# Kernel optimization log

Measured on AMD Instinct MI355X. Metric: run time of the kernel, lower is better.

The kernel has to match this reference:

```python
import jax, jax.numpy as jnp
import numpy as np

H = 1024          # hidden_size
E = 2 * H         # expansion e
S_DIM = 128       # shared q/k dim s
B, S = 4, 2048


def setup_inputs() -> dict:
    key = jax.random.key(0)
    ks = jax.random.split(key, 6)
    inputs = jax.random.normal(ks[0], (B, S, H), dtype=jnp.float32)
    W_uv = jax.random.normal(ks[1], (H, 2 * E + S_DIM), dtype=jnp.float32) * (1.0 / np.sqrt(H))
    b_uv = jnp.zeros((2 * E + S_DIM,), dtype=jnp.float32)
    gamma = jax.random.normal(ks[2], (2, S_DIM), dtype=jnp.float32) * 0.02
    beta = jnp.zeros((2, S_DIM), dtype=jnp.float32)
    W_out = jax.random.normal(ks[3], (E, H), dtype=jnp.float32) * (1.0 / np.sqrt(E))
    b_out = jnp.zeros((H,), dtype=jnp.float32)
    return {"inputs": inputs, "W_uv": W_uv, "b_uv": b_uv,
            "gamma": gamma, "beta": beta, "W_out": W_out, "b_out": b_out}


def reference(inputs, W_uv, b_uv, gamma, beta, W_out, b_out):
    seq_len = inputs.shape[1]
    # uv projection + SiLU
    uvb = jax.nn.silu(jnp.einsum('bsh,hf->bsf', inputs, W_uv) + b_uv)
    u = uvb[..., :E]                       # [B,S,E]
    v = uvb[..., E:2 * E]                  # [B,S,E]
    base = uvb[..., 2 * E:]                # [B,S,s]
    # per-head affine: [B,S,1,s]*[2,s] + [2,s] -> [B,S,2,s]
    qk = base[..., None, :] * gamma + beta
    q, k = qk[..., 0, :], qk[..., 1, :]    # [B,S,s] each
    scores = jnp.einsum('bns,bms->bnm', q, k) / seq_len   # [B,S,S]
    sq = jnp.square(jax.nn.relu(scores))
    attn_v = jnp.einsum('bnm,bme->bne', sq, v)            # [B,S,E]
    return jnp.einsum('bne,eh->bnh', u * attn_v, W_out) + b_out
```

## Files before the change

kernel.cpp:

```cpp
#include <hip/hip_runtime.h>
#include <stdint.h>


#define H_DIM  1024
#define E_DIM  2048
#define SD     128
#define B_SZ   4
#define S_LEN  2048
#define M_TOT  (B_SZ * S_LEN)
#define F_DIM  (2 * E_DIM + SD)

typedef _Float16 f16;
typedef __attribute__((ext_vector_type(4))) _Float16 f16x4;
typedef __attribute__((ext_vector_type(8))) _Float16 f16x8;
typedef __attribute__((ext_vector_type(16))) float f32x16;

__device__ __forceinline__ float silu_f(float x) { return x / (1.f + __expf(-x)); }

__device__ __forceinline__ void gload16(const void* g, void* l) {
  __builtin_amdgcn_global_load_lds(
      (const __attribute__((address_space(1))) void*)(uintptr_t)g,
      (__attribute__((address_space(3))) void*)(uint32_t)(uintptr_t)l,
      16, 0, 0);
}

__global__ __launch_bounds__(256) void cast_f16_k(const float* __restrict__ src,
                                                  f16* __restrict__ dst, long n) {
  long i = ((long)blockIdx.x * 256 + threadIdx.x) * 4;
  if (i < n) {
    float4 v = *(const float4*)(src + i);
    f16x4 h; h[0] = (f16)v.x; h[1] = (f16)v.y; h[2] = (f16)v.z; h[3] = (f16)v.w;
    *(f16x4*)(dst + i) = h;
  }
}

__global__ __launch_bounds__(256) void transpose_cast_k(const float* __restrict__ src,
                                                        f16* __restrict__ dst, int R, int C) {
  __shared__ float tile[32][33];
  int c0 = blockIdx.x * 32, r0 = blockIdx.y * 32;
  int tx = threadIdx.x & 31, ty = threadIdx.x >> 5;
  for (int i = ty; i < 32; i += 8) tile[i][tx] = src[(long)(r0 + i) * C + c0 + tx];
  __syncthreads();
  for (int i = ty; i < 32; i += 8) dst[(long)(c0 + i) * R + r0 + tx] = (f16)tile[tx][i];
}

template <int MODE>
__global__ __launch_bounds__(512, 2) void gemm256(
    const f16* __restrict__ Ag, const f16* __restrict__ Bg,
    float* __restrict__ F0, f16* __restrict__ O0, f16* __restrict__ O1,
    const f16* __restrict__ I0, const float* __restrict__ C0)
{
  constexpr int K  = (MODE == 0) ? H_DIM : (MODE == 1) ? SD : 2048;
  constexpr int NT = K / 64;

  __shared__ f16 As[2][256][64];
  __shared__ f16 Bs[2][256][64];

  const int t    = threadIdx.x;
  const int w    = t >> 6;
  const int lane = t & 63;
  const int lo5  = lane & 31;
  const int hi   = lane >> 5;
  const int wm   = w >> 2;
  const int wn   = w & 3;

  const int gx  = gridDim.x;
  const int nwg = gx * gridDim.y;
  const int lin = blockIdx.y * gx + blockIdx.x;
  const int cpx = nwg >> 3;
  const int wg  = (lin & 7) * cpx + (lin >> 3);
  const int n0  = (wg % gx) * 256;
  const int m0  = (wg / gx) * 256;
  const long z  = blockIdx.z;

  const f16* A = Ag + (MODE == 2 ? z * (long)S_LEN * S_LEN
                     : MODE == 1 ? z * (long)S_LEN * SD : 0);
  const f16* B = Bg + (MODE == 2 ? z * (long)E_DIM * S_LEN
                     : MODE == 1 ? z * (long)S_LEN * SD : 0);

  auto stageA = [&](int bb, int half, int kt2) {
    const f16* g0 = A + (long)(m0 + half * 128) * K + kt2 * 64;
    f16* lb = &As[bb][half * 128][0];
#pragma unroll
    for (int j = 0; j < 2; j++) {
      int grp = (j << 3) + w;
      int rl  = (grp << 3) + (lane >> 3);
      gload16(g0 + (long)rl * K + (((lane & 7) ^ (lane >> 3) ^ (grp & 1)) << 3),
              lb + (grp << 9));
    }
  };
  auto stageB = [&](int bb, int half, int kt2) {
    const f16* g0 = B + (long)(n0 + half * 128) * K + kt2 * 64;
    f16* lb = &Bs[bb][half * 128][0];
#pragma unroll
    for (int j = 0; j < 2; j++) {
      int grp = (j << 3) + w;
      int rl  = (grp << 3) + (lane >> 3);
      gload16(g0 + (long)rl * K + (((lane & 7) ^ (lane >> 3) ^ (grp & 1)) << 3),
              lb + (grp << 9));
    }
  };

  f32x16 acc[4][2] = {};
  f16x8 a0[2][4], a1[2][4], b0[4], b1[4];

  const int swz = (lo5 & 7) ^ ((lo5 >> 3) & 1);
  const int rA  = wm * 64 + lo5;
  const int rB  = wn * 32 + lo5;

  stageA(0, 0, 0); stageA(0, 1, 0); stageB(0, 0, 0); stageB(0, 1, 0);
  stageA(1, 0, 1); stageA(1, 1, 1); stageB(1, 0, 1); stageB(1, 1, 1);
  asm volatile("s_waitcnt vmcnt(8)" ::: "memory");
  __builtin_amdgcn_s_barrier();

  for (int kt = 0; kt < NT; ++kt) {
    const int bf = kt & 1;
    const bool s2 = (kt + 2 < NT);

#pragma unroll
    for (int ksl = 0; ksl < 4; ksl++) {
      const int pc = ((((ksl << 1) + hi) ^ swz) << 3);
      a0[0][ksl] = *(const f16x8*)&As[bf][rA][pc];
      a0[1][ksl] = *(const f16x8*)&As[bf][rA + 32][pc];
      b0[ksl]    = *(const f16x8*)&Bs[bf][rB][pc];
    }
    __builtin_amdgcn_s_barrier();
    __builtin_amdgcn_s_setprio(1);
#pragma unroll
    for (int ksl = 0; ksl < 4; ksl++) {
      acc[0][0] = __builtin_amdgcn_mfma_f32_32x32x16_f16(a0[0][ksl], b0[ksl], acc[0][0], 0, 0, 0);
      acc[0][1] = __builtin_amdgcn_mfma_f32_32x32x16_f16(a0[1][ksl], b0[ksl], acc[0][1], 0, 0, 0);
    }
    __builtin_amdgcn_s_setprio(0);
    __builtin_amdgcn_s_barrier();

    if (s2) { stageA(bf, 0, kt + 2); stageB(bf, 0, kt + 2); }
#pragma unroll
    for (int ksl = 0; ksl < 4; ksl++) {
      const int pc = ((((ksl << 1) + hi) ^ swz) << 3);
      b1[ksl] = *(const f16x8*)&Bs[bf][128 + rB][pc];
    }
    __builtin_amdgcn_s_barrier();
    __builtin_amdgcn_s_setprio(1);
#pragma unroll
    for (int ksl = 0; ksl < 4; ksl++) {
      acc[1][0] = __builtin_amdgcn_mfma_f32_32x32x16_f16(a0[0][ksl], b1[ksl], acc[1][0], 0, 0, 0);
      acc[1][1] = __builtin_amdgcn_mfma_f32_32x32x16_f16(a0[1][ksl], b1[ksl], acc[1][1], 0, 0, 0);
    }
    __builtin_amdgcn_s_setprio(0);
    __builtin_amdgcn_s_barrier();

    if (s2) stageB(bf, 1, kt + 2);
#pragma unroll
    for (int ksl = 0; ksl < 4; ksl++) {
      const int pc = ((((ksl << 1) + hi) ^ swz) << 3);
      a1[0][ksl] = *(const f16x8*)&As[bf][128 + rA][pc];
      a1[1][ksl] = *(const f16x8*)&As[bf][128 + rA + 32][pc];
    }
    __builtin_amdgcn_s_barrier();
    __builtin_amdgcn_s_setprio(1);
#pragma unroll
    for (int ksl = 0; ksl < 4; ksl++) {
      acc[3][0] = __builtin_amdgcn_mfma_f32_32x32x16_f16(a1[0][ksl], b1[ksl], acc[3][0], 0, 0, 0);
      acc[3][1] = __builtin_amdgcn_mfma_f32_32x32x16_f16(a1[1][ksl], b1[ksl], acc[3][1], 0, 0, 0);
    }
    __builtin_amdgcn_s_setprio(0);
    __builtin_amdgcn_s_barrier();

    if (s2) stageA(bf, 1, kt + 2);
    __builtin_amdgcn_s_barrier();
    __builtin_amdgcn_s_setprio(1);
#pragma unroll
    for (int ksl = 0; ksl < 4; ksl++) {
      acc[2][0] = __builtin_amdgcn_mfma_f32_32x32x16_f16(a1[0][ksl], b0[ksl], acc[2][0], 0, 0, 0);
      acc[2][1] = __builtin_amdgcn_mfma_f32_32x32x16_f16(a1[1][ksl], b0[ksl], acc[2][1], 0, 0, 0);
    }
    __builtin_amdgcn_s_setprio(0);
    if (s2) { asm volatile("s_waitcnt vmcnt(8)" ::: "memory"); }
    else    { asm volatile("s_waitcnt vmcnt(0)" ::: "memory"); }
    __builtin_amdgcn_s_barrier();
  }

#pragma unroll
  for (int q = 0; q < 4; q++) {
    const int ms = q >> 1;
    const int ns = q & 1;
#pragma unroll
    for (int im = 0; im < 2; im++) {
      const int gc    = n0 + ns * 128 + wn * 32 + lo5;
      const int rbase = m0 + ms * 128 + wm * 64 + im * 32 + (hi << 2);
      if (MODE == 0) {
        const float bias = C0[gc];
        if (n0 < E_DIM) {
#pragma unroll
          for (int g = 0; g < 4; g++)
#pragma unroll
            for (int rr = 0; rr < 4; rr++) {
              int gr = rbase + (g << 3) + rr;
              O0[(long)gr * E_DIM + gc] = (f16)silu_f(acc[q][im][g * 4 + rr] + bias);
            }
        } else {
#pragma unroll
          for (int g = 0; g < 4; g++) {
            int gr0 = rbase + (g << 3);
            int b   = gr0 >> 11;
            int s0  = gr0 & (S_LEN - 1);
            f16x4 pk;
#pragma unroll
            for (int rr = 0; rr < 4; rr++) pk[rr] = (f16)silu_f(acc[q][im][g * 4 + rr] + bias);
            *(f16x4*)&O1[((long)b * E_DIM + (gc - E_DIM)) * S_LEN + s0] = pk;
          }
        }
      } else if (MODE == 1) {
        const long base = z * (long)S_LEN * S_LEN;
#pragma unroll
        for (int g = 0; g < 4; g++)
#pragma unroll
          for (int rr = 0; rr < 4; rr++) {
            int gr = rbase + (g << 3) + rr;
            float tv = fmaxf(acc[q][im][g * 4 + rr], 0.f) * 64.f;
            O0[base + (long)gr * S_LEN + gc] = (f16)(tv * tv);
          }
      } else if (MODE == 2) {
        const long rowoff = z * S_LEN;
#pragma unroll
        for (int g = 0; g < 4; g++)
#pragma unroll
          for (int rr = 0; rr < 4; rr++) {
            int gr = rbase + (g << 3) + rr;
            long idx = (rowoff + gr) * (long)E_DIM + gc;
            O0[idx] = (f16)((float)I0[idx] * acc[q][im][g * 4 + rr]);
          }
      } else {
        const float bias = C0[gc];
#pragma unroll
        for (int g = 0; g < 4; g++)
#pragma unroll
          for (int rr = 0; rr < 4; rr++) {
            int gr = rbase + (g << 3) + rr;
            F0[(long)gr * H_DIM + gc] = acc[q][im][g * 4 + rr] * (1.0f / 17179869184.0f) + bias;
          }
      }
    }
  }
}

template <int MODE>
__global__ __launch_bounds__(256) void mfma_gemm(
    const f16* __restrict__ Ag, const f16* __restrict__ Bg,
    float* __restrict__ F0, f16* __restrict__ H0, const f16* __restrict__ H1,
    f16* __restrict__ H2, f16* __restrict__ H3,
    const float* __restrict__ C0, const float* __restrict__ C1,
    const float* __restrict__ C2)
{
  constexpr int K   = (MODE == 1) ? SD : H_DIM;
  constexpr int LDA = K, LDB = K;

  __shared__ f16 As[2][128][32];
  __shared__ f16 Bs[2][128][32];

  const int t    = threadIdx.x;
  const int w    = t >> 6;
  const int lane = t & 63;
  const int lo5  = lane & 31;
  const int hi   = lane >> 5;
  const int wy   = w >> 1, wx = w & 1;
  const int m0   = blockIdx.y * 128;
  const int n0   = blockIdx.x * 128;
  const long z   = blockIdx.z;

  const f16* A = Ag + (MODE == 1 ? z * (long)S_LEN * SD : 0);
  const f16* B = Bg + (MODE == 1 ? z * (long)S_LEN * SD : 0);

  const int srow = lane >> 2;
  const int scol = (((lane & 3) ^ ((srow >> 1) & 3))) * 8;
  const int rsw  = (lo5 >> 1) & 3;

  f32x16 acc[2][2] = {};

  for (int k0 = 0; k0 < K; k0 += 64) {
#pragma unroll
    for (int h = 0; h < 2; h++)
#pragma unroll
      for (int g16 = 0; g16 < 2; g16++) {
        const int r = (w << 5) + (g16 << 4);
        gload16(A + (long)(m0 + r + srow) * LDA + k0 + (h << 5) + scol, &As[h][r][0]);
        gload16(B + (long)(n0 + r + srow) * LDB + k0 + (h << 5) + scol, &Bs[h][r][0]);
      }
    __syncthreads();

#pragma unroll
    for (int ks = 0; ks < 4; ks++) {
      const int h  = ks >> 1;
      const int cl = ((ks & 1) << 1) + hi;
      const int kc = (cl ^ rsw) << 3;
      f16x8 av[2], bv[2];
#pragma unroll
      for (int i = 0; i < 2; i++)
        av[i] = *(const f16x8*)&As[h][(wy << 6) + (i << 5) + lo5][kc];
#pragma unroll
      for (int j = 0; j < 2; j++)
        bv[j] = *(const f16x8*)&Bs[h][(wx << 6) + (j << 5) + lo5][kc];
#pragma unroll
      for (int i = 0; i < 2; i++)
#pragma unroll
        for (int j = 0; j < 2; j++)
          acc[i][j] = __builtin_amdgcn_mfma_f32_32x32x16_f16(av[i], bv[j], acc[i][j], 0, 0, 0);
    }
    __syncthreads();
  }

  const int rb0 = m0 + (wy << 6) + (hi << 2);
  const int cb0 = n0 + (wx << 6) + lo5;

  if (MODE == 4) {
#pragma unroll
    for (int i = 0; i < 2; i++)
#pragma unroll
      for (int j = 0; j < 2; j++) {
        int jj = cb0 + (j << 5);
        float bias = C0[jj];
        float g0 = C1[jj], g1 = C1[SD + jj];
        float be0 = C2[jj], be1 = C2[SD + jj];
#pragma unroll
        for (int g = 0; g < 4; g++)
#pragma unroll
          for (int rr = 0; rr < 4; rr++) {
            int gr = rb0 + (i << 5) + (g << 3) + rr;
            float s = silu_f(acc[i][j][g * 4 + rr] + bias);
            H2[(long)gr * SD + jj] = (f16)(s * g0 + be0);
            H3[(long)gr * SD + jj] = (f16)(s * g1 + be1);
          }
      }
  } else {
#pragma unroll
    for (int i = 0; i < 2; i++)
#pragma unroll
      for (int j = 0; j < 2; j++) {
        int gc = cb0 + (j << 5);
#pragma unroll
        for (int g = 0; g < 4; g++)
#pragma unroll
          for (int rr = 0; rr < 4; rr++) {
            int gr = rb0 + (i << 5) + (g << 3) + rr;
            float tv = fmaxf(acc[i][j][g * 4 + rr], 0.f) * 64.f;
            H0[z * (long)S_LEN * S_LEN + (long)gr * S_LEN + gc] = (f16)(tv * tv);
          }
      }
  }
}

extern "C" void kernel_launch(void* const* d_in, const int* in_sizes, int n_in,
                              void* d_out, int out_size, void* d_ws, size_t ws_size,
                              hipStream_t stream) {
  const float* X     = (const float*)d_in[0];
  const float* W_uv  = (const float*)d_in[1];
  const float* b_uv  = (const float*)d_in[2];
  const float* gamma = (const float*)d_in[3];
  const float* beta  = (const float*)d_in[4];
  const float* W_out = (const float*)d_in[5];
  const float* b_out = (const float*)d_in[6];
  float* out = (float*)d_out;

  char* wp = (char*)d_ws;
  f16* Xh   = (f16*)wp; wp += (long)M_TOT * H_DIM * 2;
  f16* Wuvt = (f16*)wp; wp += (long)F_DIM * H_DIM * 2;
  f16* Wt   = (f16*)wp; wp += (long)H_DIM * E_DIM * 2;
  f16* u    = (f16*)wp; wp += (long)M_TOT * E_DIM * 2;
  f16* vt   = (f16*)wp; wp += (long)M_TOT * E_DIM * 2;
  f16* qh   = (f16*)wp; wp += (long)M_TOT * SD * 2;
  f16* kh   = (f16*)wp; wp += (long)M_TOT * SD * 2;
  f16* sq   = (f16*)wp; wp += (long)B_SZ * S_LEN * S_LEN * 2;
  f16* p    = (f16*)wp; wp += (long)M_TOT * E_DIM * 2;

  cast_f16_k<<<(M_TOT * H_DIM) / (256 * 4), 256, 0, stream>>>(X, Xh, (long)M_TOT * H_DIM);
  transpose_cast_k<<<dim3(F_DIM / 32, H_DIM / 32), 256, 0, stream>>>(W_uv, Wuvt, H_DIM, F_DIM);
  transpose_cast_k<<<dim3(H_DIM / 32, E_DIM / 32), 256, 0, stream>>>(W_out, Wt, E_DIM, H_DIM);

  gemm256<0><<<dim3(2 * E_DIM / 256, M_TOT / 256, 1), 512, 0, stream>>>(
      Xh, Wuvt, nullptr, u, vt, nullptr, b_uv);

  mfma_gemm<4><<<dim3(1, M_TOT / 128, 1), 256, 0, stream>>>(
      Xh, Wuvt + (long)2 * E_DIM * H_DIM, nullptr, nullptr, nullptr, qh, kh,
      b_uv + 2 * E_DIM, gamma, beta);

  gemm256<1><<<dim3(S_LEN / 256, S_LEN / 256, B_SZ), 512, 0, stream>>>(
      qh, kh, nullptr, sq, nullptr, nullptr, nullptr);

  gemm256<2><<<dim3(E_DIM / 256, S_LEN / 256, B_SZ), 512, 0, stream>>>(
      sq, vt, nullptr, p, nullptr, u, nullptr);

  gemm256<3><<<dim3(H_DIM / 256, M_TOT / 256, 1), 512, 0, stream>>>(
      p, Wt, out, nullptr, nullptr, nullptr, b_out);
}
```

Measured before the change: 384.9 us.

## Fuse q/k projection into uv GEMM and split-K the output GEMM

Extends the uv projection GEMM with an extra column tile that computes the shared base projection and writes q and k with the per-head affine. This removes the separate small-tile GEMM launch. The final output GEMM is split into two K halves across grid z: one half writes to the output with bias, the other to a scratch buffer. A vector add kernel then combines them. This fills more CUs in the final GEMM at the cost of an extra full-output read/write pass and wasted padding work in the extra tile.

```diff
diff --git a/kernel.cpp b/kernel.cpp
--- a/kernel.cpp
+++ b/kernel.cpp
@@ -44,14 +44,26 @@
   for (int i = ty; i < 32; i += 8) dst[(long)(c0 + i) * R + r0 + tx] = (f16)tile[tx][i];
 }
 
+__global__ __launch_bounds__(256) void addf4_k(float* __restrict__ dst,
+                                               const float* __restrict__ src) {
+  long i = ((long)blockIdx.x * 256 + threadIdx.x) * 4;
+  float4 a = *(const float4*)(dst + i);
+  float4 b = *(const float4*)(src + i);
+  a.x += b.x; a.y += b.y; a.z += b.z; a.w += b.w;
+  *(float4*)(dst + i) = a;
+}
+
 template <int MODE>
 __global__ __launch_bounds__(512, 2) void gemm256(
     const f16* __restrict__ Ag, const f16* __restrict__ Bg,
     float* __restrict__ F0, f16* __restrict__ O0, f16* __restrict__ O1,
-    const f16* __restrict__ I0, const float* __restrict__ C0)
+    const f16* __restrict__ I0, const float* __restrict__ C0,
+    const float* __restrict__ C1, const float* __restrict__ C2,
+    f16* __restrict__ Q0, f16* __restrict__ K0)
 {
-  constexpr int K  = (MODE == 0) ? H_DIM : (MODE == 1) ? SD : 2048;
-  constexpr int NT = K / 64;
+  constexpr int KE = (MODE == 0) ? H_DIM : (MODE == 1) ? SD : (MODE == 2) ? 2048 : 1024;
+  constexpr int LD = (MODE == 3) ? 2048 : KE;
+  constexpr int NT = KE / 64;
 
   __shared__ f16 As[2][256][64];
   __shared__ f16 Bs[2][256][64];
@@ -74,29 +86,33 @@
   const long z  = blockIdx.z;
 
   const f16* A = Ag + (MODE == 2 ? z * (long)S_LEN * S_LEN
-                     : MODE == 1 ? z * (long)S_LEN * SD : 0);
+                     : MODE == 1 ? z * (long)S_LEN * SD
+                     : MODE == 3 ? z * 1024 : 0);
   const f16* B = Bg + (MODE == 2 ? z * (long)E_DIM * S_LEN
-                     : MODE == 1 ? z * (long)S_LEN * SD : 0);
+                     : MODE == 1 ? z * (long)S_LEN * SD
+                     : MODE == 3 ? z * 1024 : 0);
 
   auto stageA = [&](int bb, int half, int kt2) {
-    const f16* g0 = A + (long)(m0 + half * 128) * K + kt2 * 64;
+    const f16* g0 = A + (long)(m0 + half * 128) * LD + kt2 * 64;
     f16* lb = &As[bb][half * 128][0];
 #pragma unroll
     for (int j = 0; j < 2; j++) {
       int grp = (j << 3) + w;
       int rl  = (grp << 3) + (lane >> 3);
-      gload16(g0 + (long)rl * K + (((lane & 7) ^ (lane >> 3) ^ (grp & 1)) << 3),
+      gload16(g0 + (long)rl * LD + (((lane & 7) ^ (lane >> 3) ^ (grp & 1)) << 3),
               lb + (grp << 9));
     }
   };
   auto stageB = [&](int bb, int half, int kt2) {
-    const f16* g0 = B + (long)(n0 + half * 128) * K + kt2 * 64;
     f16* lb = &Bs[bb][half * 128][0];
 #pragma unroll
     for (int j = 0; j < 2; j++) {
       int grp = (j << 3) + w;
       int rl  = (grp << 3) + (lane >> 3);
-      gload16(g0 + (long)rl * K + (((lane & 7) ^ (lane >> 3) ^ (grp & 1)) << 3),
+      int grow = n0 + half * 128 + rl;
+      if (MODE == 0) grow = min(grow, F_DIM - 1);
+      gload16(B + (long)grow * LD + kt2 * 64 +
+                  (((lane & 7) ^ (lane >> 3) ^ (grp & 1)) << 3),
               lb + (grp << 9));
     }
   };
@@ -190,8 +206,8 @@
       const int gc    = n0 + ns * 128 + wn * 32 + lo5;
       const int rbase = m0 + ms * 128 + wm * 64 + im * 32 + (hi << 2);
       if (MODE == 0) {
-        const float bias = C0[gc];
         if (n0 < E_DIM) {
+          const float bias = C0[gc];
 #pragma unroll
           for (int g = 0; g < 4; g++)
 #pragma unroll
@@ -199,7 +215,8 @@
               int gr = rbase + (g << 3) + rr;
               O0[(long)gr * E_DIM + gc] = (f16)silu_f(acc[q][im][g * 4 + rr] + bias);
             }
-        } else {
+        } else if (n0 < 2 * E_DIM) {
+          const float bias = C0[gc];
 #pragma unroll
           for (int g = 0; g < 4; g++) {
             int gr0 = rbase + (g << 3);
@@ -210,6 +227,22 @@
             for (int rr = 0; rr < 4; rr++) pk[rr] = (f16)silu_f(acc[q][im][g * 4 + rr] + bias);
             *(f16x4*)&O1[((long)b * E_DIM + (gc - E_DIM)) * S_LEN + s0] = pk;
           }
+        } else {
+          int jj = gc - 2 * E_DIM;
+          if (jj < SD) {
+            float bias = C0[gc];
+            float g0 = C1[jj], g1 = C1[SD + jj];
+            float be0 = C2[jj], be1 = C2[SD + jj];
+#pragma unroll
+            for (int g = 0; g < 4; g++)
+#pragma unroll
+              for (int rr = 0; rr < 4; rr++) {
+                int gr = rbase + (g << 3) + rr;
+                float s = silu_f(acc[q][im][g * 4 + rr] + bias);
+                Q0[(long)gr * SD + jj] = (f16)(s * g0 + be0);
+                K0[(long)gr * SD + jj] = (f16)(s * g1 + be1);
+              }
+          }
         }
       } else if (MODE == 1) {
         const long base = z * (long)S_LEN * S_LEN;
@@ -232,121 +265,17 @@
             O0[idx] = (f16)((float)I0[idx] * acc[q][im][g * 4 + rr]);
           }
       } else {
-        const float bias = C0[gc];
+        float* dst = (z == 0) ? F0 : (float*)O1;
+        const float bias = (z == 0) ? C0[gc] : 0.f;
 #pragma unroll
         for (int g = 0; g < 4; g++)
 #pragma unroll
           for (int rr = 0; rr < 4; rr++) {
             int gr = rbase + (g << 3) + rr;
-            F0[(long)gr * H_DIM + gc] = acc[q][im][g * 4 + rr] * (1.0f / 17179869184.0f) + bias;
+            dst[(long)gr * H_DIM + gc] = acc[q][im][g * 4 + rr] * (1.0f / 17179869184.0f) + bias;
           }
       }
     }
-  }
-}
-
-template <int MODE>
-__global__ __launch_bounds__(256) void mfma_gemm(
-    const f16* __restrict__ Ag, const f16* __restrict__ Bg,
-    float* __restrict__ F0, f16* __restrict__ H0, const f16* __restrict__ H1,
-    f16* __restrict__ H2, f16* __restrict__ H3,
-    const float* __restrict__ C0, const float* __restrict__ C1,
-    const float* __restrict__ C2)
-{
-  constexpr int K   = (MODE == 1) ? SD : H_DIM;
-  constexpr int LDA = K, LDB = K;
-
-  __shared__ f16 As[2][128][32];
-  __shared__ f16 Bs[2][128][32];
-
-  const int t    = threadIdx.x;
-  const int w    = t >> 6;
-  const int lane = t & 63;
-  const int lo5  = lane & 31;
-  const int hi   = lane >> 5;
-  const int wy   = w >> 1, wx = w & 1;
-  const int m0   = blockIdx.y * 128;
-  const int n0   = blockIdx.x * 128;
-  const long z   = blockIdx.z;
-
-  const f16* A = Ag + (MODE == 1 ? z * (long)S_LEN * SD : 0);
-  const f16* B = Bg + (MODE == 1 ? z * (long)S_LEN * SD : 0);
-
-  const int srow = lane >> 2;
-  const int scol = (((lane & 3) ^ ((srow >> 1) & 3))) * 8;
-  const int rsw  = (lo5 >> 1) & 3;
-
-  f32x16 acc[2][2] = {};
-
-  for (int k0 = 0; k0 < K; k0 += 64) {
-#pragma unroll
-    for (int h = 0; h < 2; h++)
-#pragma unroll
-      for (int g16 = 0; g16 < 2; g16++) {
-        const int r = (w << 5) + (g16 << 4);
-        gload16(A + (long)(m0 + r + srow) * LDA + k0 + (h << 5) + scol, &As[h][r][0]);
-        gload16(B + (long)(n0 + r + srow) * LDB + k0 + (h << 5) + scol, &Bs[h][r][0]);
-      }
-    __syncthreads();
-
-#pragma unroll
-    for (int ks = 0; ks < 4; ks++) {
-      const int h  = ks >> 1;
-      const int cl = ((ks & 1) << 1) + hi;
-      const int kc = (cl ^ rsw) << 3;
-      f16x8 av[2], bv[2];
-#pragma unroll
-      for (int i = 0; i < 2; i++)
-        av[i] = *(const f16x8*)&As[h][(wy << 6) + (i << 5) + lo5][kc];
-#pragma unroll
-      for (int j = 0; j < 2; j++)
-        bv[j] = *(const f16x8*)&Bs[h][(wx << 6) + (j << 5) + lo5][kc];
-#pragma unroll
-      for (int i = 0; i < 2; i++)
-#pragma unroll
-        for (int j = 0; j < 2; j++)
-          acc[i][j] = __builtin_amdgcn_mfma_f32_32x32x16_f16(av[i], bv[j], acc[i][j], 0, 0, 0);
-    }
-    __syncthreads();
-  }
-
-  const int rb0 = m0 + (wy << 6) + (hi << 2);
-  const int cb0 = n0 + (wx << 6) + lo5;
-
-  if (MODE == 4) {
-#pragma unroll
-    for (int i = 0; i < 2; i++)
-#pragma unroll
-      for (int j = 0; j < 2; j++) {
-        int jj = cb0 + (j << 5);
-        float bias = C0[jj];
-        float g0 = C1[jj], g1 = C1[SD + jj];
-        float be0 = C2[jj], be1 = C2[SD + jj];
-#pragma unroll
-        for (int g = 0; g < 4; g++)
-#pragma unroll
-          for (int rr = 0; rr < 4; rr++) {
-            int gr = rb0 + (i << 5) + (g << 3) + rr;
-            float s = silu_f(acc[i][j][g * 4 + rr] + bias);
-            H2[(long)gr * SD + jj] = (f16)(s * g0 + be0);
-            H3[(long)gr * SD + jj] = (f16)(s * g1 + be1);
-          }
-      }
-  } else {
-#pragma unroll
-    for (int i = 0; i < 2; i++)
-#pragma unroll
-      for (int j = 0; j < 2; j++) {
-        int gc = cb0 + (j << 5);
-#pragma unroll
-        for (int g = 0; g < 4; g++)
-#pragma unroll
-          for (int rr = 0; rr < 4; rr++) {
-            int gr = rb0 + (i << 5) + (g << 3) + rr;
-            float tv = fmaxf(acc[i][j][g * 4 + rr], 0.f) * 64.f;
-            H0[z * (long)S_LEN * S_LEN + (long)gr * S_LEN + gc] = (f16)(tv * tv);
-          }
-      }
   }
 }
 
@@ -377,19 +306,17 @@
   transpose_cast_k<<<dim3(F_DIM / 32, H_DIM / 32), 256, 0, stream>>>(W_uv, Wuvt, H_DIM, F_DIM);
   transpose_cast_k<<<dim3(H_DIM / 32, E_DIM / 32), 256, 0, stream>>>(W_out, Wt, E_DIM, H_DIM);
 
-  gemm256<0><<<dim3(2 * E_DIM / 256, M_TOT / 256, 1), 512, 0, stream>>>(
-      Xh, Wuvt, nullptr, u, vt, nullptr, b_uv);
-
-  mfma_gemm<4><<<dim3(1, M_TOT / 128, 1), 256, 0, stream>>>(
-      Xh, Wuvt + (long)2 * E_DIM * H_DIM, nullptr, nullptr, nullptr, qh, kh,
-      b_uv + 2 * E_DIM, gamma, beta);
+  gemm256<0><<<dim3(17, M_TOT / 256, 1), 512, 0, stream>>>(
+      Xh, Wuvt, nullptr, u, vt, nullptr, b_uv, gamma, beta, qh, kh);
 
   gemm256<1><<<dim3(S_LEN / 256, S_LEN / 256, B_SZ), 512, 0, stream>>>(
-      qh, kh, nullptr, sq, nullptr, nullptr, nullptr);
+      qh, kh, nullptr, sq, nullptr, nullptr, nullptr, nullptr, nullptr, nullptr, nullptr);
 
   gemm256<2><<<dim3(E_DIM / 256, S_LEN / 256, B_SZ), 512, 0, stream>>>(
-      sq, vt, nullptr, p, nullptr, u, nullptr);
-
-  gemm256<3><<<dim3(H_DIM / 256, M_TOT / 256, 1), 512, 0, stream>>>(
-      p, Wt, out, nullptr, nullptr, nullptr, b_out);
-}
+      sq, vt, nullptr, p, nullptr, u, nullptr, nullptr, nullptr, nullptr, nullptr);
+
+  gemm256<3><<<dim3(H_DIM / 256, M_TOT / 256, 2), 512, 0, stream>>>(
+      p, Wt, out, nullptr, (f16*)u, nullptr, b_out, nullptr, nullptr, nullptr, nullptr);
+
+  addf4_k<<<(M_TOT * H_DIM) / (256 * 4), 256, 0, stream>>>(out, (const float*)u);
+}
```

New measurement: 392.7 us. 2.0% more time.

## Split-K the output projection GEMM across two z-slices with separate add pass

Applied to the files above, without the earlier changes.

The final GEMM (M=8192, N=1024, K=2048) is split along K into two halves via blockIdx.z, doubling the workgroup count from 128 to 256 so more CUs are occupied. The second half writes fp32 partials into the reused u buffer, and a new elementwise kernel adds them into the output. The price is an extra 32MB of fp32 traffic and one more launch. It also deletes an unused MODE!=4 epilogue branch in mfma_gemm.

```diff
diff --git a/kernel.cpp b/kernel.cpp
--- a/kernel.cpp
+++ b/kernel.cpp
@@ -44,14 +44,24 @@
   for (int i = ty; i < 32; i += 8) dst[(long)(c0 + i) * R + r0 + tx] = (f16)tile[tx][i];
 }
 
+__global__ __launch_bounds__(256) void addf4_k(float* __restrict__ dst,
+                                               const float* __restrict__ src) {
+  long i = ((long)blockIdx.x * 256 + threadIdx.x) * 4;
+  float4 a = *(const float4*)(dst + i);
+  float4 b = *(const float4*)(src + i);
+  a.x += b.x; a.y += b.y; a.z += b.z; a.w += b.w;
+  *(float4*)(dst + i) = a;
+}
+
 template <int MODE>
 __global__ __launch_bounds__(512, 2) void gemm256(
     const f16* __restrict__ Ag, const f16* __restrict__ Bg,
     float* __restrict__ F0, f16* __restrict__ O0, f16* __restrict__ O1,
     const f16* __restrict__ I0, const float* __restrict__ C0)
 {
-  constexpr int K  = (MODE == 0) ? H_DIM : (MODE == 1) ? SD : 2048;
-  constexpr int NT = K / 64;
+  constexpr int KE = (MODE == 0) ? H_DIM : (MODE == 1) ? SD : (MODE == 2) ? 2048 : 1024;
+  constexpr int LD = (MODE == 3) ? 2048 : KE;
+  constexpr int NT = KE / 64;
 
   __shared__ f16 As[2][256][64];
   __shared__ f16 Bs[2][256][64];
@@ -74,29 +84,31 @@
   const long z  = blockIdx.z;
 
   const f16* A = Ag + (MODE == 2 ? z * (long)S_LEN * S_LEN
-                     : MODE == 1 ? z * (long)S_LEN * SD : 0);
+                     : MODE == 1 ? z * (long)S_LEN * SD
+                     : MODE == 3 ? z * 1024 : 0);
   const f16* B = Bg + (MODE == 2 ? z * (long)E_DIM * S_LEN
-                     : MODE == 1 ? z * (long)S_LEN * SD : 0);
+                     : MODE == 1 ? z * (long)S_LEN * SD
+                     : MODE == 3 ? z * 1024 : 0);
 
   auto stageA = [&](int bb, int half, int kt2) {
-    const f16* g0 = A + (long)(m0 + half * 128) * K + kt2 * 64;
+    const f16* g0 = A + (long)(m0 + half * 128) * LD + kt2 * 64;
     f16* lb = &As[bb][half * 128][0];
 #pragma unroll
     for (int j = 0; j < 2; j++) {
       int grp = (j << 3) + w;
       int rl  = (grp << 3) + (lane >> 3);
-      gload16(g0 + (long)rl * K + (((lane & 7) ^ (lane >> 3) ^ (grp & 1)) << 3),
+      gload16(g0 + (long)rl * LD + (((lane & 7) ^ (lane >> 3) ^ (grp & 1)) << 3),
               lb + (grp << 9));
     }
   };
   auto stageB = [&](int bb, int half, int kt2) {
-    const f16* g0 = B + (long)(n0 + half * 128) * K + kt2 * 64;
+    const f16* g0 = B + (long)(n0 + half * 128) * LD + kt2 * 64;
     f16* lb = &Bs[bb][half * 128][0];
 #pragma unroll
     for (int j = 0; j < 2; j++) {
       int grp = (j << 3) + w;
       int rl  = (grp << 3) + (lane >> 3);
-      gload16(g0 + (long)rl * K + (((lane & 7) ^ (lane >> 3) ^ (grp & 1)) << 3),
+      gload16(g0 + (long)rl * LD + (((lane & 7) ^ (lane >> 3) ^ (grp & 1)) << 3),
               lb + (grp << 9));
     }
   };
@@ -232,13 +244,14 @@
             O0[idx] = (f16)((float)I0[idx] * acc[q][im][g * 4 + rr]);
           }
       } else {
-        const float bias = C0[gc];
+        float* dst = (z == 0) ? F0 : (float*)O1;
+        const float bias = (z == 0) ? C0[gc] : 0.f;
 #pragma unroll
         for (int g = 0; g < 4; g++)
 #pragma unroll
           for (int rr = 0; rr < 4; rr++) {
             int gr = rbase + (g << 3) + rr;
-            F0[(long)gr * H_DIM + gc] = acc[q][im][g * 4 + rr] * (1.0f / 17179869184.0f) + bias;
+            dst[(long)gr * H_DIM + gc] = acc[q][im][g * 4 + rr] * (1.0f / 17179869184.0f) + bias;
           }
       }
     }
@@ -330,21 +343,6 @@
             float s = silu_f(acc[i][j][g * 4 + rr] + bias);
             H2[(long)gr * SD + jj] = (f16)(s * g0 + be0);
             H3[(long)gr * SD + jj] = (f16)(s * g1 + be1);
-          }
-      }
-  } else {
-#pragma unroll
-    for (int i = 0; i < 2; i++)
-#pragma unroll
-      for (int j = 0; j < 2; j++) {
-        int gc = cb0 + (j << 5);
-#pragma unroll
-        for (int g = 0; g < 4; g++)
-#pragma unroll
-          for (int rr = 0; rr < 4; rr++) {
-            int gr = rb0 + (i << 5) + (g << 3) + rr;
-            float tv = fmaxf(acc[i][j][g * 4 + rr], 0.f) * 64.f;
-            H0[z * (long)S_LEN * S_LEN + (long)gr * S_LEN + gc] = (f16)(tv * tv);
           }
       }
   }
@@ -390,6 +388,8 @@
   gemm256<2><<<dim3(E_DIM / 256, S_LEN / 256, B_SZ), 512, 0, stream>>>(
       sq, vt, nullptr, p, nullptr, u, nullptr);
 
-  gemm256<3><<<dim3(H_DIM / 256, M_TOT / 256, 1), 512, 0, stream>>>(
-      p, Wt, out, nullptr, nullptr, nullptr, b_out);
-}
+  gemm256<3><<<dim3(H_DIM / 256, M_TOT / 256, 2), 512, 0, stream>>>(
+      p, Wt, out, nullptr, (f16*)u, nullptr, b_out);
+
+  addf4_k<<<(M_TOT * H_DIM) / (256 * 4), 256, 0, stream>>>(out, (const float*)u);
+}
```

Result: slower. 414.1 us (+7.6%).
